# Optimization experiments

Hardware: AMD Instinct MI355X
Metric: run time of the kernel (lower is better)

The kernel has to match this reference:

```python
import jax, jax.numpy as jnp
import numpy as np

B, N, K = 2, 8192, 9
FEAT_C, COST_C, FLOW_C = 128, 64, 3
CH = [128, 128]          # PointConv output channels
MLP = [128, 64]          # pointwise Conv1d channels
WN = 16                  # WeightNet output width
HID = [8, 8]             # WeightNet hidden widths
SLOPE = 0.1              # leaky relu slope
EPS = 1e-5
CLAMP = (-200.0, 200.0)


def setup_inputs() -> dict:
    key = jax.random.key(0)
    ks = iter(jax.random.split(key, 64))
    def nrm(shape, s=0.02):
        return jax.random.normal(next(ks), shape, jnp.float32) * s
    inp = {}
    inp["xyz"] = jax.random.normal(next(ks), (B, N, 3), jnp.float32)
    inp["feats"] = jax.random.normal(next(ks), (B, FEAT_C, N), jnp.float32)
    inp["cost_volume"] = jax.random.normal(next(ks), (B, COST_C, N), jnp.float32)
    inp["flow"] = jax.random.normal(next(ks), (B, FLOW_C, N), jnp.float32)
    last = FEAT_C + COST_C + FLOW_C
    for i, co in enumerate(CH):
        cin = last + 3
        p = f"pc{i}_"
        inp[p + "w1"] = nrm((HID[0], 3)); inp[p + "b1"] = jnp.zeros((HID[0],), jnp.float32)
        inp[p + "w2"] = nrm((HID[1], HID[0])); inp[p + "b2"] = jnp.zeros((HID[1],), jnp.float32)
        inp[p + "w3"] = nrm((WN, HID[1])); inp[p + "b3"] = jnp.zeros((WN,), jnp.float32)
        inp[p + "linW"] = nrm((co, cin * WN)); inp[p + "linb"] = jnp.zeros((co,), jnp.float32)
        last = co
    for i, co in enumerate(MLP):
        inp[f"mlp{i}_W"] = nrm((co, last)); inp[f"mlp{i}_b"] = jnp.zeros((co,), jnp.float32)
        last = co
    inp["fc_W"] = nrm((3, last)); inp["fc_b"] = jnp.zeros((3,), jnp.float32)
    return inp


def _bn(x, axes):
    m = x.mean(axes, keepdims=True)
    v = x.var(axes, keepdims=True)
    return (x - m) / jnp.sqrt(v + EPS)


def _leaky(x):
    return jnp.where(x >= 0, x, SLOPE * x)


def _knn_idx(xyz, k):
    # xyz: [B,N,3] -> idx [B,N,K] of k nearest (incl. self)
    sq = jnp.sum(xyz * xyz, -1)                       # [B,N]
    d = sq[:, :, None] + sq[:, None, :] - 2.0 * jnp.einsum('bnc,bmc->bnm', xyz, xyz)
    return jax.lax.top_k(-d, k)[1]                    # [B,N,K]


def _gather(a, idx):
    # a: [B,N,C], idx: [B,N,K] -> [B,N,K,C]
    return jax.vmap(lambda x, i: x[i])(a, idx)


def _pointconv(xyz, points, idx, w1, b1, w2, b2, w3, b3, linW, linb):
    # xyz [B,N,3], points [B,C,N] -> [B,out,N]
    g_xyz = _gather(xyz, idx) - xyz[:, :, None, :]    # [B,N,K,3] relative coords
    g_pts = _gather(jnp.transpose(points, (0, 2, 1)), idx)  # [B,N,K,C]
    grouped = jnp.concatenate([g_pts, g_xyz], -1)     # [B,N,K,C+3]
    # WeightNet on relative coords: 3 -> 8 -> 8 -> 16 (bn+relu each)
    h = jax.nn.relu(_bn(g_xyz @ w1.T + b1, (0, 1, 2)))
    h = jax.nn.relu(_bn(h @ w2.T + b2, (0, 1, 2)))
    w = jax.nn.relu(_bn(h @ w3.T + b3, (0, 1, 2)))    # [B,N,K,WN]
    bsz, n = grouped.shape[0], grouped.shape[1]
    agg = jnp.einsum('bnkc,bnkw->bncw', grouped, w).reshape(bsz, n, -1)
    out = agg @ linW.T + linb                         # [B,N,out]
    out = _leaky(_bn(out, (0, 1)))
    return jnp.transpose(out, (0, 2, 1))              # [B,out,N]


def reference(xyz, feats, cost_volume, flow,
              pc0_w1, pc0_b1, pc0_w2, pc0_b2, pc0_w3, pc0_b3, pc0_linW, pc0_linb,
              pc1_w1, pc1_b1, pc1_w2, pc1_b2, pc1_w3, pc1_b3, pc1_linW, pc1_linb,
              mlp0_W, mlp0_b, mlp1_W, mlp1_b, fc_W, fc_b):
    idx = _knn_idx(xyz, K)
    x = jnp.concatenate([feats, cost_volume, flow], axis=1)  # [B, feat+cost+flow, N]
    x = _pointconv(xyz, x, idx, pc0_w1, pc0_b1, pc0_w2, pc0_b2, pc0_w3, pc0_b3, pc0_linW, pc0_linb)
    x = _pointconv(xyz, x, idx, pc1_w1, pc1_b1, pc1_w2, pc1_b2, pc1_w3, pc1_b3, pc1_linW, pc1_linb)
    x = _leaky(jnp.einsum('oc,bcn->bon', mlp0_W, x) + mlp0_b[None, :, None])
    x = _leaky(jnp.einsum('oc,bcn->bon', mlp1_W, x) + mlp1_b[None, :, None])
    fl = jnp.einsum('oc,bcn->bon', fc_W, x) + fc_b[None, :, None]
    return x, jnp.clip(fl, CLAMP[0], CLAMP[1])
```

## Files before the change

### kernel.cpp

```cpp
#include <hip/hip_runtime.h>

#define NBATCH 2
#define NPTS   8192
#define NPT    (NBATCH*NPTS)
#define KNN    9
#define SEG    16
#define SEGN   (NPTS/SEG)
#define SCAP   16
#define SSTR   17

typedef unsigned short u16;
typedef unsigned int   u32;
typedef short bf16x8 __attribute__((ext_vector_type(8)));
typedef float f32x4  __attribute__((ext_vector_type(4)));

__device__ __forceinline__ float wred(float v){
#pragma unroll
  for(int o=32;o>0;o>>=1) v += __shfl_down(v,o);
  return v;
}

__device__ __forceinline__ u16 f2b(float f){
  u32 u = __float_as_uint(f);
  return (u16)((u + 0x7fffu + ((u>>16)&1u)) >> 16);
}

__device__ __forceinline__ float bumpup(float x){
  u32 u = __float_as_uint(x);
  if(u == 0x80000000u) u = 1u;
  else if((int)u >= 0) u += 1u;
  else u -= 1u;
  return __uint_as_float(u);
}

__global__ __launch_bounds__(256) void k_build_xin(
    const float* __restrict__ feats, const float* __restrict__ cost,
    const float* __restrict__ flow, float* __restrict__ xin)
{
  __shared__ float buf[196][67];
  int t = threadIdx.x;
  int pt0 = blockIdx.x*64;
  int b = pt0 >> 13, n0 = pt0 & (NPTS-1);
  int lane = t & 63, grp = t >> 6;
  const float* f  = feats + (size_t)b*128*NPTS + n0 + lane;
  const float* cv = cost  + (size_t)b*64 *NPTS + n0 + lane;
  const float* fl = flow  + (size_t)b*3  *NPTS + n0 + lane;
  for(int c=grp; c<128; c+=4) buf[c][lane]      = f[(size_t)c*NPTS];
  for(int c=grp; c<64;  c+=4) buf[128+c][lane]  = cv[(size_t)c*NPTS];
  if(grp<3) buf[192+grp][lane] = fl[(size_t)grp*NPTS];
  else      buf[195][lane] = 0.f;
  __syncthreads();
  for(int e=t; e<64*49; e+=256){
    int p = e/49, q = e-p*49;
    float4 v = make_float4(buf[4*q][p], buf[4*q+1][p], buf[4*q+2][p], buf[4*q+3][p]);
    *(float4*)(xin + (size_t)(pt0+p)*196 + 4*q) = v;
  }
}

__global__ __launch_bounds__(256) void k_thr(
    const float* __restrict__ xyz, float* __restrict__ thr)
{
  __shared__ float md[4][64][9];
  int t = threadIdx.x, lane = t & 63, wave = t >> 6;
  int qb = blockIdx.x;
  int b = qb >> 7;
  int n = (qb & 127)*64 + lane;
  const float* xb = xyz + (size_t)b*NPTS*3;
  float qx=xb[3*n], qy=xb[3*n+1], qz=xb[3*n+2];
  float qs = __fadd_rn(__fadd_rn(__fmul_rn(qx,qx),__fmul_rn(qy,qy)),__fmul_rn(qz,qz));
  float bd[KNN];
#pragma unroll
  for(int i=0;i<KNN;i++) bd[i]=__builtin_inff();
  for(int i=0;i<128;i++){
    int m = (wave*128 + i)*16;
    float cx=xb[3*m], cy=xb[3*m+1], cz=xb[3*m+2];
    float s = __fadd_rn(__fadd_rn(__fmul_rn(cx,cx),__fmul_rn(cy,cy)),__fmul_rn(cz,cz));
    float dot = fmaf(cz,qz, fmaf(cy,qy, __fmul_rn(cx,qx)));
    float d = __fsub_rn(__fadd_rn(qs,s), __fmul_rn(2.0f,dot));
    if(d < bd[KNN-1]){
      bd[KNN-1]=d;
#pragma unroll
      for(int r=KNN-2;r>=0;r--){
        if(bd[r+1] < bd[r]){ float td=bd[r]; bd[r]=bd[r+1]; bd[r+1]=td; }
      }
    }
  }
#pragma unroll
  for(int i=0;i<KNN;i++) md[wave][lane][i]=bd[i];
  __syncthreads();
  if(t < 64){
    float b2[KNN];
#pragma unroll
    for(int i=0;i<KNN;i++) b2[i]=__builtin_inff();
    for(int w=0;w<4;w++){
#pragma unroll
      for(int i=0;i<KNN;i++){
        float d = md[w][t][i];
        if(d < b2[KNN-1]){
          b2[KNN-1]=d;
#pragma unroll
          for(int r=KNN-2;r>=0;r--){
            if(b2[r+1] < b2[r]){ float td=b2[r]; b2[r]=b2[r+1]; b2[r+1]=td; }
          }
        }
      }
    }
    thr[(b<<13) + (qb & 127)*64 + t] = b2[KNN-1];
  }
}

__global__ __launch_bounds__(256) void k_knn_part(
    const float* __restrict__ xyz, const float* __restrict__ thr,
    float* __restrict__ pd, int* __restrict__ pi)
{
  __shared__ float4 cbuf[256];
  __shared__ float sdq[256*SSTR];
  __shared__ int   sqi[256*SSTR];
  int t = threadIdx.x;
  int seg = blockIdx.x & (SEG-1);
  int qc  = blockIdx.x >> 4;
  int b = qc >> 5;
  int n = (qc & 31)*256 + t;
  int pt = (b<<13) + t + (qc&31)*256;
  pt = (b<<13) + n;
  const float* xb = xyz + (size_t)b*NPTS*3;
  float qx=xb[3*n], qy=xb[3*n+1], qz=xb[3*n+2];
  float qs = __fadd_rn(__fadd_rn(__fmul_rn(qx,qx),__fmul_rn(qy,qy)),__fmul_rn(qz,qz));
  float init = bumpup(thr[pt]);
  float bd[KNN]; int bi[KNN];
#pragma unroll
  for(int i=0;i<KNN;i++){ bd[i]=init; bi[i]=0x7fffffff; }
  float cut = init;
  int cnt = 0;
  float* msd = sdq + t*SSTR;
  int*   msi = sqi + t*SSTR;
  auto flush = [&](){
    for(int i=0;i<cnt;i++){
      float d = msd[i]; int id = msi[i];
      if(d < bd[KNN-1]){
        bd[KNN-1]=d; bi[KNN-1]=id;
#pragma unroll
        for(int r=KNN-2;r>=0;r--){
          if(bd[r+1] < bd[r]){
            float td=bd[r]; bd[r]=bd[r+1]; bd[r+1]=td;
            int ti=bi[r]; bi[r]=bi[r+1]; bi[r+1]=ti;
          }
        }
      }
    }
    cnt = 0;
    cut = bd[KNN-1];
  };
  const int m0 = seg*SEGN;
  for(int tt=0; tt<SEGN; tt+=256){
    int m = m0 + tt + t;
    float cx=xb[3*m], cy=xb[3*m+1], cz=xb[3*m+2];
    float s = __fadd_rn(__fadd_rn(__fmul_rn(cx,cx),__fmul_rn(cy,cy)),__fmul_rn(cz,cz));
    cbuf[t] = make_float4(cx,cy,cz,s);
    __syncthreads();
    for(int j0=0; j0<256; j0+=8){
      float dv[8];
#pragma unroll
      for(int u=0;u<8;u++){
        float4 c = cbuf[j0+u];
        float dot = fmaf(c.z,qz, fmaf(c.y,qy, __fmul_rn(c.x,qx)));
        dv[u] = __fsub_rn(__fadd_rn(qs,c.w), __fmul_rn(2.0f,dot));
      }
#pragma unroll
      for(int u=0;u<8;u++){
        msd[cnt] = dv[u];
        msi[cnt] = m0+tt+j0+u;
        cnt += (dv[u] < cut) ? 1 : 0;
      }
      if(cnt > 8) flush();
    }
    __syncthreads();
  }
  flush();
  size_t base = ((size_t)pt*SEG + seg)*KNN;
#pragma unroll
  for(int i=0;i<KNN;i++){ pd[base+i]=bd[i]; pi[base+i]=bi[i]; }
}

__global__ __launch_bounds__(256) void k_knn_merge(
    const float* __restrict__ xyz,
    const float* __restrict__ pd, const int* __restrict__ pi,
    int* __restrict__ idxo, float* __restrict__ gpart)
{
  __shared__ float red[4][9];
  int t = threadIdx.x;
  int pt = blockIdx.x*256 + t;
  int b = pt >> 13, n = pt & (NPTS-1);
  const float* xb = xyz + (size_t)b*NPTS*3;
  const float4* dp = (const float4*)(pd + (size_t)pt*SEG*KNN);
  const int4*   ip = (const int4*)(pi + (size_t)pt*SEG*KNN);
  float bd[KNN]; int bi[KNN];
#pragma unroll
  for(int i=0;i<KNN;i++){ bd[i]=__builtin_inff(); bi[i]=0x7fffffff; }
  for(int v=0; v<SEG*KNN/4; v++){
    float4 dv = dp[v];
    int4   iv = ip[v];
    float dd[4] = {dv.x,dv.y,dv.z,dv.w};
    int   ii[4] = {iv.x,iv.y,iv.z,iv.w};
#pragma unroll
    for(int u=0;u<4;u++){
      float d = dd[u]; int id = ii[u];
      if(d < bd[KNN-1]){
        bd[KNN-1]=d; bi[KNN-1]=id;
#pragma unroll
        for(int i=KNN-2;i>=0;i--){
          if(bd[i+1] < bd[i]){
            float td=bd[i]; bd[i]=bd[i+1]; bd[i+1]=td;
            int ti=bi[i]; bi[i]=bi[i+1]; bi[i+1]=ti;
          }
        }
      }
    }
  }
#pragma unroll
  for(int r=0;r<KNN;r++) idxo[pt*KNN + r] = bi[r];
  float q0=xb[3*n], q1=xb[3*n+1], q2=xb[3*n+2];
  float mom[9];
#pragma unroll
  for(int i=0;i<9;i++) mom[i]=0.f;
#pragma unroll
  for(int r=0;r<KNN;r++){
    int m = bi[r];
    float gx=xb[3*m]-q0, gy=xb[3*m+1]-q1, gz=xb[3*m+2]-q2;
    mom[0]+=gx; mom[1]+=gy; mom[2]+=gz;
    mom[3]=fmaf(gx,gx,mom[3]); mom[4]=fmaf(gy,gy,mom[4]); mom[5]=fmaf(gz,gz,mom[5]);
    mom[6]=fmaf(gx,gy,mom[6]); mom[7]=fmaf(gx,gz,mom[7]); mom[8]=fmaf(gy,gz,mom[8]);
  }
  int wave = t>>6, lane = t&63;
#pragma unroll
  for(int i=0;i<9;i++){
    float s = wred(mom[i]);
    if(lane==0) red[wave][i]=s;
  }
  __syncthreads();
  if(t<9)
    gpart[blockIdx.x*9 + t] = red[0][t]+red[1][t]+red[2][t]+red[3][t];
}

__global__ __launch_bounds__(256) void k_wn23a(
    const float* __restrict__ xyz, const int* __restrict__ idx,
    const float* __restrict__ gpart, float cnt,
    const float* __restrict__ W1, const float* __restrict__ B1,
    const float* __restrict__ W2, const float* __restrict__ B2,
    float* __restrict__ hout, float* __restrict__ partialOut)
{
  __shared__ float mom[9];
  __shared__ float stl[16];
  int t = threadIdx.x;
  if(t<9){
    float s=0.f;
    for(int r=0;r<64;r++) s += gpart[r*9+t];
    mom[t]=s;
  }
  __syncthreads();
  if(t<8){
    float inv = 1.0f/cnt;
    float w0=W1[3*t], w1=W1[3*t+1], w2=W1[3*t+2], bb=B1[t];
    float Eg0=mom[0]*inv, Eg1=mom[1]*inv, Eg2=mom[2]*inv;
    float Mxx=mom[3]*inv, Myy=mom[4]*inv, Mzz=mom[5]*inv;
    float Mxy=mom[6]*inv, Mxz=mom[7]*inv, Myz=mom[8]*inv;
    float mu_lin = w0*Eg0 + w1*Eg1 + w2*Eg2;
    float mean = mu_lin + bb;
    float e2 = w0*w0*Mxx + w1*w1*Myy + w2*w2*Mzz
             + 2.f*(w0*w1*Mxy + w0*w2*Mxz + w1*w2*Myz)
             + 2.f*bb*mu_lin + bb*bb;
    float var = e2 - mean*mean;
    stl[t] = mean;
    stl[8+t] = 1.0f/sqrtf(var + 1e-5f);
  }
  __syncthreads();
  int e = blockIdx.x*256 + t;
  int pt = e/KNN;
  int b = pt>>13, n = pt & (NPTS-1);
  int m = idx[e];
  const float* xb = xyz + (size_t)b*NPTS*3;
  float gx = xb[3*m]-xb[3*n], gy = xb[3*m+1]-xb[3*n+1], gz = xb[3*m+2]-xb[3*n+2];
  float x[8];
#pragma unroll
  for(int j=0;j<8;j++){
    float d = fmaf(gz, W1[3*j+2], fmaf(gy, W1[3*j+1], gx*W1[3*j]));
    float v = d + B1[j];
    v = (v - stl[j])*stl[8+j];
    x[j] = v>0.f? v : 0.f;
  }
  float v[8];
#pragma unroll
  for(int j=0;j<8;j++){
    float d = 0.f;
#pragma unroll
    for(int i=0;i<8;i++) d = fmaf(x[i], W2[j*8+i], d);
    v[j] = d + B2[j];
    hout[(size_t)e*8 + j] = v[j];
  }
  __shared__ float red[4][2][8];
  int wave = t>>6, lane = t&63;
#pragma unroll
  for(int j=0;j<8;j++){
    float s = wred(v[j]);
    float q = wred(v[j]*v[j]);
    if(lane==0){ red[wave][0][j]=s; red[wave][1][j]=q; }
  }
  __syncthreads();
  if(t < 16){
    int isq = t>>3, c = t&7;
    partialOut[blockIdx.x*16 + t] =
      red[0][isq][c]+red[1][isq][c]+red[2][isq][c]+red[3][isq][c];
  }
}

template<int CI, int CO>
__global__ __launch_bounds__(256) void k_wn23(
    const float* __restrict__ hin, const float* __restrict__ partialIn,
    int nb, float cnt,
    const float* __restrict__ W, const float* __restrict__ Bv,
    float* __restrict__ hout, float* __restrict__ partialOut)
{
  __shared__ float sa[256], qa[256];
  __shared__ float stl[2*CI];
  int t = threadIdx.x;
  {
    int c = t % CI;
    int r0 = t / CI;
    int stride = 256 / CI;
    float s=0.f, q=0.f;
    for(int r=r0; r<nb; r+=stride){
      s += partialIn[r*2*CI + c];
      q += partialIn[r*2*CI + CI + c];
    }
    sa[t]=s; qa[t]=q;
    __syncthreads();
    if(t < CI){
      for(int g=1; g<stride; g++){ s += sa[t+g*CI]; q += qa[t+g*CI]; }
      float mean = s/cnt;
      float var  = q/cnt - mean*mean;
      stl[t]    = mean;
      stl[CI+t] = 1.0f/sqrtf(var + 1e-5f);
    }
    __syncthreads();
  }
  int e = blockIdx.x*256 + t;
  float x[CI];
#pragma unroll
  for(int i=0;i<CI;i++){
    float v = (hin[(size_t)e*CI + i] - stl[i])*stl[CI+i];
    x[i] = v>0.f? v : 0.f;
  }
  float v[CO];
#pragma unroll
  for(int j=0;j<CO;j++){
    float d = 0.f;
#pragma unroll
    for(int i=0;i<CI;i++) d = fmaf(x[i], W[j*CI+i], d);
    v[j] = d + Bv[j];
    hout[(size_t)e*CO + j] = v[j];
  }
  __shared__ float red[4][2][CO];
  int wave = t>>6, lane = t&63;
#pragma unroll
  for(int j=0;j<CO;j++){
    float s = wred(v[j]);
    float q = wred(v[j]*v[j]);
    if(lane==0){ red[wave][0][j]=s; red[wave][1][j]=q; }
  }
  __syncthreads();
  if(t < 2*CO){
    int isq = t/CO, c = t%CO;
    partialOut[blockIdx.x*2*CO + t] =
      red[0][isq][c]+red[1][isq][c]+red[2][isq][c]+red[3][isq][c];
  }
}

__global__ __launch_bounds__(256) void k_fin(
    const float* __restrict__ partial, float* __restrict__ st,
    int C, int nb, float cnt)
{
  __shared__ float sa[256], qa[256];
  int t = threadIdx.x;
  int c = t % C;
  int r0 = t / C;
  int stride = 256 / C;
  float s=0.f, q=0.f;
  for(int r=r0; r<nb; r+=stride){
    s += partial[r*2*C + c];
    q += partial[r*2*C + C + c];
  }
  sa[t]=s; qa[t]=q;
  __syncthreads();
  if(t < C){
    for(int g=1; g<stride; g++){ s += sa[t+g*C]; q += qa[t+g*C]; }
    float mean = s/cnt;
    float var  = q/cnt - mean*mean;
    st[t]   = mean;
    st[C+t] = 1.0f/sqrtf(var + 1e-5f);
  }
}

__global__ __launch_bounds__(256) void k_prepW(
    const float* __restrict__ linW, u16* __restrict__ Wh, int AW, int KP)
{
  int e = blockIdx.x*256 + threadIdx.x;
  if(e >= 128*KP) return;
  int o = e / KP, k = e - o*KP;
  float w = (k < AW) ? linW[o*AW + k] : 0.f;
  Wh[e] = f2b(w);
}

template<int CIN, int XSTRIDE, int KP, bool BN>
__global__ __launch_bounds__(256) void k_buildA(
    const float* __restrict__ xin, const float* __restrict__ xyz,
    const int* __restrict__ idx, const float* __restrict__ wpre,
    const float* __restrict__ st3, const float* __restrict__ bnst,
    u16* __restrict__ Abuf, int c0)
{
  constexpr int P = 16;
  constexpr int CPTS = CIN-3;
  constexpr int CPAD = KP/16;
  __shared__ float wm[P][KNN][16];
  __shared__ float gxs[P][KNN][3];
  __shared__ int   si[P][KNN];
  __shared__ float sm3[16], sr3[16];
  int t = threadIdx.x;
  int pt0 = c0 + blockIdx.x*P;
  int b = pt0 >> 13;
  const float* xb = xyz + (size_t)b*NPTS*3;
  if(t<16){ sm3[t]=st3[t]; sr3[t]=st3[16+t]; }
  for(int e=t; e<P*KNN; e+=256){
    int p = e/KNN, k = e - p*KNN;
    int n = (pt0+p)&(NPTS-1);
    int m = idx[(pt0+p)*KNN+k];
    si[p][k]=m;
    gxs[p][k][0]=xb[3*m]  -xb[3*n];
    gxs[p][k][1]=xb[3*m+1]-xb[3*n+1];
    gxs[p][k][2]=xb[3*m+2]-xb[3*n+2];
  }
  __syncthreads();
  for(int e=t; e<P*KNN*16; e+=256){
    int p = e/(KNN*16); int r = e - p*(KNN*16); int k = r>>4, wn = r&15;
    float v = (wpre[((size_t)(pt0+p)*KNN + k)*16 + wn] - sm3[wn]) * sr3[wn];
    wm[p][k][wn] = v>0.f? v:0.f;
  }
  __syncthreads();
  for(int it=t; it<P*CPAD; it+=256){
    int p = it/CPAD, c = it - p*CPAD;
    u32 u[8];
    if(c < CIN){
      float g[KNN];
      if(c < CPTS){
#pragma unroll
        for(int k=0;k<KNN;k++)
          g[k] = xin[(size_t)((b<<13) + si[p][k])*XSTRIDE + c];
        if(BN){
          float sm = bnst[c], sr = bnst[128+c];
#pragma unroll
          for(int k=0;k<KNN;k++){
            float v = (g[k]-sm)*sr;
            g[k] = v>=0.f? v : 0.1f*v;
          }
        }
      } else {
        int cc = c - CPTS;
#pragma unroll
        for(int k=0;k<KNN;k++) g[k] = gxs[p][k][cc];
      }
      float a[16];
#pragma unroll
      for(int wn=0; wn<16; wn++){
        float s = 0.f;
#pragma unroll
        for(int k=0;k<KNN;k++) s = fmaf(g[k], wm[p][k][wn], s);
        a[wn] = s;
      }
#pragma unroll
      for(int j=0;j<8;j++)
        u[j] = (u32)f2b(a[2*j]) | ((u32)f2b(a[2*j+1])<<16);
    } else {
#pragma unroll
      for(int j=0;j<8;j++) u[j]=0;
    }
    u32* dst = (u32*)(Abuf + ((size_t)(blockIdx.x*P + p)*KP + c*16));
    *(uint4*)dst       = make_uint4(u[0],u[1],u[2],u[3]);
    *((uint4*)dst + 1) = make_uint4(u[4],u[5],u[6],u[7]);
  }
}

__device__ __forceinline__ void gload16(const void* g, void* l){
  __builtin_amdgcn_global_load_lds(
      (const __attribute__((address_space(1))) u32*)g,
      (__attribute__((address_space(3))) u32*)l, 16, 0, 0);
}

template<int KP>
__global__ __launch_bounds__(512) void k_gemm(
    const u16* __restrict__ Wh, const u16* __restrict__ A,
    const float* __restrict__ linb, float* __restrict__ outp,
    float* __restrict__ partial, int ptBase)
{
  __shared__ __attribute__((aligned(16))) u16 lds[24576];
  constexpr int NT = KP/64;
  int t = threadIdx.x, wave = t>>6, lane = t&63;
  int p0 = blockIdx.x*64;
  const u16* Ab = A + (size_t)p0*KP;

  auto stage = [&](const u16* __restrict__ g, int k0, int ldsByteOff, int rows){
    int nr = (rows*128) >> 13;
    for(int r=0;r<nr;r++){
      int y  = (r*8 + wave) << 10;
      int yl = y + lane*16;
      int row = yl >> 7;
      int s = (yl >> 4) & 7;
      int c = s ^ (row & 7);
      const u16* src = g + (size_t)row*KP + k0 + c*8;
      gload16(src, (char*)lds + ldsByteOff + y);
    }
  };

  stage(Wh, 0, 0,     128);
  stage(Ab, 0, 32768, 64);

  f32x4 acc[4];
#pragma unroll
  for(int j=0;j<4;j++) acc[j]=(f32x4)(0.f);

  for(int kt=0; kt<NT; kt++){
    int cur = kt & 1;
    __syncthreads();
    if(kt+1 < NT){
      int nxt = cur^1;
      stage(Wh, (kt+1)*64, nxt*16384,         128);
      stage(Ab, (kt+1)*64, 32768 + nxt*8192,  64);
    }
    const u16* Lw = lds + cur*8192;
    const u16* La = lds + 16384 + cur*4096;
#pragma unroll
    for(int kf=0; kf<2; kf++){
      int cb = kf*4 + (lane>>4);
      bf16x8 af[4];
#pragma unroll
      for(int nf=0; nf<4; nf++){
        int p = nf*16 + (lane&15);
        af[nf] = *(const bf16x8*)(La + p*64 + ((cb ^ (p&7))<<3));
      }
      int row = wave*16 + (lane&15);
      bf16x8 wh = *(const bf16x8*)(Lw + row*64 + ((cb ^ (row&7))<<3));
#pragma unroll
      for(int nf=0; nf<4; nf++)
        acc[nf] = __builtin_amdgcn_mfma_f32_16x16x32_bf16(wh, af[nf], acc[nf], 0,0,0);
    }
  }

  int gb = (ptBase>>6) + blockIdx.x;
  int q = lane>>4, lc = lane&15;
  int obase = wave*16 + q*4;
#pragma unroll
  for(int r=0;r<4;r++){
    int o = obase + r;
    float bo = linb[o];
    float sv = 0.f, qv = 0.f;
#pragma unroll
    for(int nf=0; nf<4; nf++){
      float x = acc[nf][r] + bo;
      outp[(size_t)(ptBase + p0 + nf*16 + lc)*128 + o] = x;
      sv += x; qv = fmaf(x,x,qv);
    }
#pragma unroll
    for(int off=8; off>0; off>>=1){
      sv += __shfl_down(sv,off);
      qv += __shfl_down(qv,off);
    }
    if(lc==0){
      partial[gb*256 + o]       = sv;
      partial[gb*256 + 128 + o] = qv;
    }
  }
}

__global__ __launch_bounds__(512) void k_mlp(
    const float* __restrict__ outp1, const float* __restrict__ sto,
    const float* __restrict__ W0, const float* __restrict__ B0,
    const float* __restrict__ W1, const float* __restrict__ B1,
    const float* __restrict__ Wf, const float* __restrict__ Bf,
    float* __restrict__ dout)
{
  __shared__ float w0l[128*129];
  __shared__ float w1l[128*65];
  __shared__ float xt [128*65];
  __shared__ float m1l[64*65];
  int t = threadIdx.x;
  int pt0 = blockIdx.x*64;
  int b = pt0 >> 13, n0 = pt0 & (NPTS-1);
  for(int e=t; e<128*128; e+=512){ int o=e>>7, j=e&127; w0l[j*129+o] = W0[e]; }
  for(int e=t; e<64*128;  e+=512){ int o=e>>7, j=e&127; w1l[j*65+o]  = W1[e]; }
  for(int e=t; e<64*128;  e+=512){
    int p=e>>7, j=e&127;
    float v = outp1[(size_t)(pt0+p)*128 + j];
    v = (v - sto[j])*sto[128+j];
    xt[j*65+p] = v>=0.f? v : 0.1f*v;
  }
  __syncthreads();
  int p = t&63, wv = t>>6;
  float acc[16];
#pragma unroll
  for(int i=0;i<16;i++) acc[i]=0.f;
  for(int j=0;j<128;j++){
    float xv = xt[j*65+p];
#pragma unroll
    for(int i=0;i<16;i++)
      acc[i] = fmaf(w0l[j*129 + wv*16 + i], xv, acc[i]);
  }
  __syncthreads();
#pragma unroll
  for(int i=0;i<16;i++){
    int o = wv*16+i;
    float v = acc[i] + B0[o];
    v = v>=0.f? v : 0.1f*v;
    xt[o*65 + p] = v;
  }
  __syncthreads();
  float a2[8];
#pragma unroll
  for(int i=0;i<8;i++) a2[i]=0.f;
  for(int j=0;j<128;j++){
    float xv = xt[j*65+p];
#pragma unroll
    for(int i=0;i<8;i++)
      a2[i] = fmaf(w1l[j*65 + wv*8 + i], xv, a2[i]);
  }
#pragma unroll
  for(int i=0;i<8;i++){
    int o = wv*8+i;
    float v = a2[i] + B1[o];
    v = v>=0.f? v : 0.1f*v;
    dout[(size_t)(b*64+o)*NPTS + n0 + p] = v;
    m1l[o*65+p] = v;
  }
  __syncthreads();
  if(t < 192){
    int o = t/64, pp = t%64;
    float a = Bf[o];
    for(int j=0;j<64;j++) a = fmaf(Wf[o*64+j], m1l[j*65+pp], a);
    a = fminf(fmaxf(a, -200.f), 200.f);
    dout[(size_t)NBATCH*64*NPTS + (size_t)(b*3+o)*NPTS + n0 + pp] = a;
  }
}

extern "C" void kernel_launch(void* const* d_in, const int* in_sizes, int n_in,
                              void* d_out, int out_size, void* d_ws, size_t ws_size,
                              hipStream_t stream)
{
  (void)in_sizes; (void)n_in; (void)out_size;
  const float* xyz   = (const float*)d_in[0];
  const float* feats = (const float*)d_in[1];
  const float* cost  = (const float*)d_in[2];
  const float* flow  = (const float*)d_in[3];
  const float* pw1[2]  = {(const float*)d_in[4],  (const float*)d_in[12]};
  const float* pb1[2]  = {(const float*)d_in[5],  (const float*)d_in[13]};
  const float* pw2[2]  = {(const float*)d_in[6],  (const float*)d_in[14]};
  const float* pb2[2]  = {(const float*)d_in[7],  (const float*)d_in[15]};
  const float* pw3[2]  = {(const float*)d_in[8],  (const float*)d_in[16]};
  const float* pb3[2]  = {(const float*)d_in[9],  (const float*)d_in[17]};
  const float* plW[2]  = {(const float*)d_in[10], (const float*)d_in[18]};
  const float* plb[2]  = {(const float*)d_in[11], (const float*)d_in[19]};
  const float* m0W = (const float*)d_in[20];
  const float* m0b = (const float*)d_in[21];
  const float* m1W = (const float*)d_in[22];
  const float* m1b = (const float*)d_in[23];
  const float* fcW = (const float*)d_in[24];
  const float* fcb = (const float*)d_in[25];
  float* out = (float*)d_out;

  const int KP0 = 3200, AW0 = 3168;
  const int KP1 = 2112, AW1 = 2096;

  float* ws = (float*)d_ws;
  size_t o = 0;
  float* xin0 = ws + o; o += (size_t)NPT*196;
  int*   idx  = (int*)(ws + o); o += (size_t)NPT*KNN + 3;
  o &= ~(size_t)3;
  float* thr  = ws + o; o += (size_t)NPT;
  float* pd   = ws + o; o += (size_t)NPT*SEG*KNN;
  int*   pi   = (int*)(ws + o); o += (size_t)NPT*SEG*KNN;
  float* h2   = ws + o; o += (size_t)NPT*KNN*8;
  float* wpre = ws + o; o += (size_t)NPT*KNN*16;
  float* gpart = ws + o; o += 64*9 + 7;
  float* part2 = ws + o; o += 576*16;
  float* part3 = ws + o; o += 576*32;
  float* parto = ws + o; o += 65536;
  float* st3  = ws + o; o += 32;
  float* sto0 = ws + o; o += 256;
  float* sto1 = ws + o; o += 256;
  float* outp0 = ws + o; o += (size_t)NPT*128;
  float* outp1 = ws + o; o += (size_t)NPT*128;
  u16* Wh0 = (u16*)(ws + o); o += (size_t)128*KP0/2;
  u16* Wh1 = (u16*)(ws + o); o += (size_t)128*KP1/2;
  u16* Abuf = (u16*)(ws + o);
  size_t used_bytes = o*4;
  size_t avail = ws_size > used_bytes ? ws_size - used_bytes : 0;
  int npc = NPT;
  while(npc > 1024 && (size_t)npc*KP0*2 > avail) npc >>= 1;

  k_build_xin<<<NPT/64, 256, 0, stream>>>(feats, cost, flow, xin0);
  k_thr<<<256, 256, 0, stream>>>(xyz, thr);
  k_knn_part<<<64*SEG, 256, 0, stream>>>(xyz, thr, pd, pi);
  k_knn_merge<<<NPT/256, 256, 0, stream>>>(xyz, pd, pi, idx, gpart);

  k_prepW<<<(128*KP0+255)/256, 256, 0, stream>>>(plW[0], Wh0, AW0, KP0);
  k_prepW<<<(128*KP1+255)/256, 256, 0, stream>>>(plW[1], Wh1, AW1, KP1);

  const float cnt1 = (float)(NPT*KNN);
  const float cnto = (float)NPT;

  for(int L=0; L<2; ++L){
    k_wn23a<<<576,256,0,stream>>>(xyz, idx, gpart, cnt1,
                                  pw1[L], pb1[L], pw2[L], pb2[L], h2, part2);
    k_wn23<8,16><<<576,256,0,stream>>>(h2, part2, 576, cnt1, pw3[L], pb3[L], wpre, part3);
    k_fin<<<1,256,0,stream>>>(part3, st3, 16, 576, cnt1);
    for(int c0 = 0; c0 < NPT; c0 += npc){
      if(L==0){
        k_buildA<198,196,KP0,false><<<npc/16,256,0,stream>>>(xin0, xyz, idx, wpre, st3, sto0, Abuf, c0);
        k_gemm<KP0><<<npc/64,512,0,stream>>>(Wh0, Abuf, plb[0], outp0, parto, c0);
      } else {
        k_buildA<131,128,KP1,true><<<npc/16,256,0,stream>>>(outp0, xyz, idx, wpre, st3, sto0, Abuf, c0);
        k_gemm<KP1><<<npc/64,512,0,stream>>>(Wh1, Abuf, plb[1], outp1, parto, c0);
      }
    }
    k_fin<<<1,256,0,stream>>>(parto, (L==0)? sto0 : sto1, 128, NPT/64, cnto);
  }

  k_mlp<<<NPT/64,512,0,stream>>>(outp1, sto1, m0W,m0b, m1W,m1b, fcW,fcb, out);
}
```

Baseline: 566.4 us.

## Precompute packed xyz+norm, read candidates directly in KNN, batch both WeightNet layers

A new pass packs each point's coordinates and squared norm into a float4 array. The threshold and partial-KNN kernels now read from it instead of recomputing norms, and the partial KNN drops its shared-memory candidate staging and block barriers in favour of direct global (L1/L2-cached) float4 loads. Its candidate buffering also changes to append only on a hit, flushing when the buffer is full. Separately, the WeightNet stages for both PointConv layers are fused into single launches with separate buffers, cutting the number of kernel launches and small reductions from six to three.

```diff
diff --git a/kernel.cpp b/kernel.cpp
--- a/kernel.cpp
+++ b/kernel.cpp
@@ -57,26 +57,36 @@
   }
 }
 
+__global__ __launch_bounds__(256) void k_xyzs(
+    const float* __restrict__ xyz, float4* __restrict__ xs)
+{
+  int pt = blockIdx.x*256 + threadIdx.x;
+  int b = pt >> 13, n = pt & (NPTS-1);
+  const float* p = xyz + (size_t)b*NPTS*3 + 3*n;
+  float x=p[0], y=p[1], z=p[2];
+  float s = __fadd_rn(__fadd_rn(__fmul_rn(x,x),__fmul_rn(y,y)),__fmul_rn(z,z));
+  xs[pt] = make_float4(x,y,z,s);
+}
+
 __global__ __launch_bounds__(256) void k_thr(
-    const float* __restrict__ xyz, float* __restrict__ thr)
+    const float4* __restrict__ xs, float* __restrict__ thr)
 {
   __shared__ float md[4][64][9];
   int t = threadIdx.x, lane = t & 63, wave = t >> 6;
   int qb = blockIdx.x;
   int b = qb >> 7;
   int n = (qb & 127)*64 + lane;
-  const float* xb = xyz + (size_t)b*NPTS*3;
-  float qx=xb[3*n], qy=xb[3*n+1], qz=xb[3*n+2];
-  float qs = __fadd_rn(__fadd_rn(__fmul_rn(qx,qx),__fmul_rn(qy,qy)),__fmul_rn(qz,qz));
+  const float4* xb4 = xs + (size_t)b*NPTS;
+  float4 q = xb4[n];
+  float qx=q.x, qy=q.y, qz=q.z, qs=q.w;
   float bd[KNN];
 #pragma unroll
   for(int i=0;i<KNN;i++) bd[i]=__builtin_inff();
   for(int i=0;i<128;i++){
     int m = (wave*128 + i)*16;
-    float cx=xb[3*m], cy=xb[3*m+1], cz=xb[3*m+2];
-    float s = __fadd_rn(__fadd_rn(__fmul_rn(cx,cx),__fmul_rn(cy,cy)),__fmul_rn(cz,cz));
-    float dot = fmaf(cz,qz, fmaf(cy,qy, __fmul_rn(cx,qx)));
-    float d = __fsub_rn(__fadd_rn(qs,s), __fmul_rn(2.0f,dot));
+    float4 c = xb4[m];
+    float dot = fmaf(c.z,qz, fmaf(c.y,qy, __fmul_rn(c.x,qx)));
+    float d = __fsub_rn(__fadd_rn(qs,c.w), __fmul_rn(2.0f,dot));
     if(d < bd[KNN-1]){
       bd[KNN-1]=d;
 #pragma unroll
@@ -110,10 +120,9 @@
 }
 
 __global__ __launch_bounds__(256) void k_knn_part(
-    const float* __restrict__ xyz, const float* __restrict__ thr,
+    const float4* __restrict__ xs, const float* __restrict__ thr,
     float* __restrict__ pd, int* __restrict__ pi)
 {
-  __shared__ float4 cbuf[256];
   __shared__ float sdq[256*SSTR];
   __shared__ int   sqi[256*SSTR];
   int t = threadIdx.x;
@@ -121,11 +130,10 @@
   int qc  = blockIdx.x >> 4;
   int b = qc >> 5;
   int n = (qc & 31)*256 + t;
-  int pt = (b<<13) + t + (qc&31)*256;
-  pt = (b<<13) + n;
-  const float* xb = xyz + (size_t)b*NPTS*3;
-  float qx=xb[3*n], qy=xb[3*n+1], qz=xb[3*n+2];
-  float qs = __fadd_rn(__fadd_rn(__fmul_rn(qx,qx),__fmul_rn(qy,qy)),__fmul_rn(qz,qz));
+  int pt = (b<<13) + n;
+  const float4* xb4 = xs + (size_t)b*NPTS;
+  float4 q = xb4[n];
+  float qx=q.x, qy=q.y, qz=q.z, qs=q.w;
   float init = bumpup(thr[pt]);
   float bd[KNN]; int bi[KNN];
 #pragma unroll
@@ -152,29 +160,21 @@
     cut = bd[KNN-1];
   };
   const int m0 = seg*SEGN;
-  for(int tt=0; tt<SEGN; tt+=256){
-    int m = m0 + tt + t;
-    float cx=xb[3*m], cy=xb[3*m+1], cz=xb[3*m+2];
-    float s = __fadd_rn(__fadd_rn(__fmul_rn(cx,cx),__fmul_rn(cy,cy)),__fmul_rn(cz,cz));
-    cbuf[t] = make_float4(cx,cy,cz,s);
-    __syncthreads();
-    for(int j0=0; j0<256; j0+=8){
-      float dv[8];
-#pragma unroll
-      for(int u=0;u<8;u++){
-        float4 c = cbuf[j0+u];
-        float dot = fmaf(c.z,qz, fmaf(c.y,qy, __fmul_rn(c.x,qx)));
-        dv[u] = __fsub_rn(__fadd_rn(qs,c.w), __fmul_rn(2.0f,dot));
-      }
-#pragma unroll
-      for(int u=0;u<8;u++){
-        msd[cnt] = dv[u];
-        msi[cnt] = m0+tt+j0+u;
-        cnt += (dv[u] < cut) ? 1 : 0;
-      }
-      if(cnt > 8) flush();
-    }
-    __syncthreads();
+  for(int j0=0; j0<SEGN; j0+=8){
+    float dv[8];
+#pragma unroll
+    for(int u=0;u<8;u++){
+      float4 c = xb4[m0+j0+u];
+      float dot = fmaf(c.z,qz, fmaf(c.y,qy, __fmul_rn(c.x,qx)));
+      dv[u] = __fsub_rn(__fadd_rn(qs,c.w), __fmul_rn(2.0f,dot));
+    }
+#pragma unroll
+    for(int u=0;u<8;u++){
+      if(dv[u] < cut){
+        msd[cnt]=dv[u]; msi[cnt]=m0+j0+u; cnt++;
+        if(cnt==SCAP) flush();
+      }
+    }
   }
   flush();
   size_t base = ((size_t)pt*SEG + seg)*KNN;
@@ -242,15 +242,19 @@
     gpart[blockIdx.x*9 + t] = red[0][t]+red[1][t]+red[2][t]+red[3][t];
 }
 
-__global__ __launch_bounds__(256) void k_wn23a(
+__global__ __launch_bounds__(256) void k_wn23a2(
     const float* __restrict__ xyz, const int* __restrict__ idx,
     const float* __restrict__ gpart, float cnt,
-    const float* __restrict__ W1, const float* __restrict__ B1,
-    const float* __restrict__ W2, const float* __restrict__ B2,
-    float* __restrict__ hout, float* __restrict__ partialOut)
+    const float* __restrict__ W1a, const float* __restrict__ B1a,
+    const float* __restrict__ W2a, const float* __restrict__ B2a,
+    const float* __restrict__ W1b, const float* __restrict__ B1b,
+    const float* __restrict__ W2b, const float* __restrict__ B2b,
+    float* __restrict__ houta, float* __restrict__ houtb,
+    float* __restrict__ parta, float* __restrict__ partb)
 {
   __shared__ float mom[9];
-  __shared__ float stl[16];
+  __shared__ float stl[2][16];
+  __shared__ float red[4][2][8];
   int t = threadIdx.x;
   if(t<9){
     float s=0.f;
@@ -258,9 +262,12 @@
     mom[t]=s;
   }
   __syncthreads();
-  if(t<8){
+  if(t<16){
+    int L = t>>3, j = t&7;
+    const float* W1 = L? W1b : W1a;
+    const float* B1 = L? B1b : B1a;
     float inv = 1.0f/cnt;
-    float w0=W1[3*t], w1=W1[3*t+1], w2=W1[3*t+2], bb=B1[t];
+    float w0=W1[3*j], w1=W1[3*j+1], w2=W1[3*j+2], bb=B1[j];
     float Eg0=mom[0]*inv, Eg1=mom[1]*inv, Eg2=mom[2]*inv;
     float Mxx=mom[3]*inv, Myy=mom[4]*inv, Mzz=mom[5]*inv;
     float Mxy=mom[6]*inv, Mxz=mom[7]*inv, Myz=mom[8]*inv;
@@ -270,8 +277,8 @@
              + 2.f*(w0*w1*Mxy + w0*w2*Mxz + w1*w2*Myz)
              + 2.f*bb*mu_lin + bb*bb;
     float var = e2 - mean*mean;
-    stl[t] = mean;
-    stl[8+t] = 1.0f/sqrtf(var + 1e-5f);
+    stl[L][j] = mean;
+    stl[L][8+j] = 1.0f/sqrtf(var + 1e-5f);
   }
   __syncthreads();
   int e = blockIdx.x*256 + t;
@@ -280,98 +287,150 @@
   int m = idx[e];
   const float* xb = xyz + (size_t)b*NPTS*3;
   float gx = xb[3*m]-xb[3*n], gy = xb[3*m+1]-xb[3*n+1], gz = xb[3*m+2]-xb[3*n+2];
-  float x[8];
-#pragma unroll
-  for(int j=0;j<8;j++){
-    float d = fmaf(gz, W1[3*j+2], fmaf(gy, W1[3*j+1], gx*W1[3*j]));
-    float v = d + B1[j];
-    v = (v - stl[j])*stl[8+j];
-    x[j] = v>0.f? v : 0.f;
-  }
-  float v[8];
-#pragma unroll
-  for(int j=0;j<8;j++){
-    float d = 0.f;
-#pragma unroll
-    for(int i=0;i<8;i++) d = fmaf(x[i], W2[j*8+i], d);
-    v[j] = d + B2[j];
-    hout[(size_t)e*8 + j] = v[j];
-  }
-  __shared__ float red[4][2][8];
   int wave = t>>6, lane = t&63;
 #pragma unroll
-  for(int j=0;j<8;j++){
-    float s = wred(v[j]);
-    float q = wred(v[j]*v[j]);
-    if(lane==0){ red[wave][0][j]=s; red[wave][1][j]=q; }
-  }
-  __syncthreads();
-  if(t < 16){
-    int isq = t>>3, c = t&7;
-    partialOut[blockIdx.x*16 + t] =
-      red[0][isq][c]+red[1][isq][c]+red[2][isq][c]+red[3][isq][c];
-  }
-}
-
-template<int CI, int CO>
-__global__ __launch_bounds__(256) void k_wn23(
-    const float* __restrict__ hin, const float* __restrict__ partialIn,
+  for(int L=0; L<2; L++){
+    const float* W1 = L? W1b : W1a;
+    const float* B1 = L? B1b : B1a;
+    const float* W2 = L? W2b : W2a;
+    const float* B2 = L? B2b : B2a;
+    float* hout = L? houtb : houta;
+    float* part = L? partb : parta;
+    float x[8];
+#pragma unroll
+    for(int j=0;j<8;j++){
+      float d = fmaf(gz, W1[3*j+2], fmaf(gy, W1[3*j+1], gx*W1[3*j]));
+      float v = d + B1[j];
+      v = (v - stl[L][j])*stl[L][8+j];
+      x[j] = v>0.f? v : 0.f;
+    }
+    float v[8];
+#pragma unroll
+    for(int j=0;j<8;j++){
+      float d = 0.f;
+#pragma unroll
+      for(int i=0;i<8;i++) d = fmaf(x[i], W2[j*8+i], d);
+      v[j] = d + B2[j];
+      hout[(size_t)e*8 + j] = v[j];
+    }
+#pragma unroll
+    for(int j=0;j<8;j++){
+      float s = wred(v[j]);
+      float q = wred(v[j]*v[j]);
+      if(lane==0){ red[wave][0][j]=s; red[wave][1][j]=q; }
+    }
+    __syncthreads();
+    if(t < 16){
+      int isq = t>>3, c = t&7;
+      part[blockIdx.x*16 + t] =
+        red[0][isq][c]+red[1][isq][c]+red[2][isq][c]+red[3][isq][c];
+    }
+    __syncthreads();
+  }
+}
+
+__global__ __launch_bounds__(256) void k_wn23_2(
+    const float* __restrict__ hina, const float* __restrict__ pina,
+    const float* __restrict__ hinb, const float* __restrict__ pinb,
     int nb, float cnt,
-    const float* __restrict__ W, const float* __restrict__ Bv,
-    float* __restrict__ hout, float* __restrict__ partialOut)
+    const float* __restrict__ Wa, const float* __restrict__ Ba,
+    const float* __restrict__ Wb, const float* __restrict__ Bb,
+    float* __restrict__ houta, float* __restrict__ houtb,
+    float* __restrict__ parta, float* __restrict__ partb)
 {
   __shared__ float sa[256], qa[256];
-  __shared__ float stl[2*CI];
+  __shared__ float stl[16];
+  __shared__ float red[4][2][16];
   int t = threadIdx.x;
-  {
-    int c = t % CI;
-    int r0 = t / CI;
-    int stride = 256 / CI;
+  int e = blockIdx.x*256 + t;
+  int wave = t>>6, lane = t&63;
+#pragma unroll
+  for(int L=0; L<2; L++){
+    const float* hin = L? hinb : hina;
+    const float* pin = L? pinb : pina;
+    const float* W   = L? Wb : Wa;
+    const float* Bv  = L? Bb : Ba;
+    float* hout = L? houtb : houta;
+    float* part = L? partb : parta;
+    {
+      int c = t % 8;
+      int r0 = t / 8;
+      float s=0.f, q=0.f;
+      for(int r=r0; r<nb; r+=32){
+        s += pin[r*16 + c];
+        q += pin[r*16 + 8 + c];
+      }
+      sa[t]=s; qa[t]=q;
+      __syncthreads();
+      if(t < 8){
+        for(int g=1; g<32; g++){ s += sa[t+g*8]; q += qa[t+g*8]; }
+        float mean = s/cnt;
+        float var  = q/cnt - mean*mean;
+        stl[t]   = mean;
+        stl[8+t] = 1.0f/sqrtf(var + 1e-5f);
+      }
+      __syncthreads();
+    }
+    float x[8];
+#pragma unroll
+    for(int i=0;i<8;i++){
+      float v = (hin[(size_t)e*8 + i] - stl[i])*stl[8+i];
+      x[i] = v>0.f? v : 0.f;
+    }
+    float v[16];
+#pragma unroll
+    for(int j=0;j<16;j++){
+      float d = 0.f;
+#pragma unroll
+      for(int i=0;i<8;i++) d = fmaf(x[i], W[j*8+i], d);
+      v[j] = d + Bv[j];
+      hout[(size_t)e*16 + j] = v[j];
+    }
+#pragma unroll
+    for(int j=0;j<16;j++){
+      float s = wred(v[j]);
+      float q = wred(v[j]*v[j]);
+      if(lane==0){ red[wave][0][j]=s; red[wave][1][j]=q; }
+    }
+    __syncthreads();
+    if(t < 32){
+      int isq = t>>4, c = t&15;
+      part[blockIdx.x*32 + t] =
+        red[0][isq][c]+red[1][isq][c]+red[2][isq][c]+red[3][isq][c];
+    }
+    __syncthreads();
+  }
+}
+
+__global__ __launch_bounds__(256) void k_fin2(
+    const float* __restrict__ pa, const float* __restrict__ pb,
+    float* __restrict__ sta, float* __restrict__ stb, int nb, float cnt)
+{
+  __shared__ float sa[256], qa[256];
+  int t = threadIdx.x;
+  const int C = 16;
+#pragma unroll
+  for(int L=0; L<2; L++){
+    const float* partial = L? pb : pa;
+    float* st = L? stb : sta;
+    int c = t % C;
+    int r0 = t / C;
+    int stride = 256 / C;
     float s=0.f, q=0.f;
     for(int r=r0; r<nb; r+=stride){
-      s += partialIn[r*2*CI + c];
-      q += partialIn[r*2*CI + CI + c];
+      s += partial[r*2*C + c];
+      q += partial[r*2*C + C + c];
     }
     sa[t]=s; qa[t]=q;
     __syncthreads();
-    if(t < CI){
-      for(int g=1; g<stride; g++){ s += sa[t+g*CI]; q += qa[t+g*CI]; }
+    if(t < C){
+      for(int g=1; g<stride; g++){ s += sa[t+g*C]; q += qa[t+g*C]; }
       float mean = s/cnt;
       float var  = q/cnt - mean*mean;
-      stl[t]    = mean;
-      stl[CI+t] = 1.0f/sqrtf(var + 1e-5f);
+      st[t]   = mean;
+      st[C+t] = 1.0f/sqrtf(var + 1e-5f);
     }
     __syncthreads();
-  }
-  int e = blockIdx.x*256 + t;
-  float x[CI];
-#pragma unroll
-  for(int i=0;i<CI;i++){
-    float v = (hin[(size_t)e*CI + i] - stl[i])*stl[CI+i];
-    x[i] = v>0.f? v : 0.f;
-  }
-  float v[CO];
-#pragma unroll
-  for(int j=0;j<CO;j++){
-    float d = 0.f;
-#pragma unroll
-    for(int i=0;i<CI;i++) d = fmaf(x[i], W[j*CI+i], d);
-    v[j] = d + Bv[j];
-    hout[(size_t)e*CO + j] = v[j];
-  }
-  __shared__ float red[4][2][CO];
-  int wave = t>>6, lane = t&63;
-#pragma unroll
-  for(int j=0;j<CO;j++){
-    float s = wred(v[j]);
-    float q = wred(v[j]*v[j]);
-    if(lane==0){ red[wave][0][j]=s; red[wave][1][j]=q; }
-  }
-  __syncthreads();
-  if(t < 2*CO){
-    int isq = t/CO, c = t%CO;
-    partialOut[blockIdx.x*2*CO + t] =
-      red[0][isq][c]+red[1][isq][c]+red[2][isq][c]+red[3][isq][c];
   }
 }
 
@@ -681,16 +740,22 @@
   float* xin0 = ws + o; o += (size_t)NPT*196;
   int*   idx  = (int*)(ws + o); o += (size_t)NPT*KNN + 3;
   o &= ~(size_t)3;
+  float4* xs  = (float4*)(ws + o); o += (size_t)NPT*4;
   float* thr  = ws + o; o += (size_t)NPT;
   float* pd   = ws + o; o += (size_t)NPT*SEG*KNN;
   int*   pi   = (int*)(ws + o); o += (size_t)NPT*SEG*KNN;
-  float* h2   = ws + o; o += (size_t)NPT*KNN*8;
-  float* wpre = ws + o; o += (size_t)NPT*KNN*16;
+  float* h2a  = ws + o; o += (size_t)NPT*KNN*8;
+  float* h2b  = ws + o; o += (size_t)NPT*KNN*8;
+  float* wpre0 = ws + o; o += (size_t)NPT*KNN*16;
+  float* wpre1 = ws + o; o += (size_t)NPT*KNN*16;
   float* gpart = ws + o; o += 64*9 + 7;
-  float* part2 = ws + o; o += 576*16;
-  float* part3 = ws + o; o += 576*32;
+  float* part2a = ws + o; o += 576*16;
+  float* part2b = ws + o; o += 576*16;
+  float* part3a = ws + o; o += 576*32;
+  float* part3b = ws + o; o += 576*32;
   float* parto = ws + o; o += 65536;
-  float* st3  = ws + o; o += 32;
+  float* st3a = ws + o; o += 32;
+  float* st3b = ws + o; o += 32;
   float* sto0 = ws + o; o += 256;
   float* sto1 = ws + o; o += 256;
   float* outp0 = ws + o; o += (size_t)NPT*128;
@@ -704,8 +769,9 @@
   while(npc > 1024 && (size_t)npc*KP0*2 > avail) npc >>= 1;
 
   k_build_xin<<<NPT/64, 256, 0, stream>>>(feats, cost, flow, xin0);
-  k_thr<<<256, 256, 0, stream>>>(xyz, thr);
-  k_knn_part<<<64*SEG, 256, 0, stream>>>(xyz, thr, pd, pi);
+  k_xyzs<<<NPT/256, 256, 0, stream>>>(xyz, xs);
+  k_thr<<<256, 256, 0, stream>>>(xs, thr);
+  k_knn_part<<<64*SEG, 256, 0, stream>>>(xs, thr, pd, pi);
   k_knn_merge<<<NPT/256, 256, 0, stream>>>(xyz, pd, pi, idx, gpart);
 
   k_prepW<<<(128*KP0+255)/256, 256, 0, stream>>>(plW[0], Wh0, AW0, KP0);
@@ -714,22 +780,26 @@
   const float cnt1 = (float)(NPT*KNN);
   const float cnto = (float)NPT;
 
-  for(int L=0; L<2; ++L){
-    k_wn23a<<<576,256,0,stream>>>(xyz, idx, gpart, cnt1,
-                                  pw1[L], pb1[L], pw2[L], pb2[L], h2, part2);
-    k_wn23<8,16><<<576,256,0,stream>>>(h2, part2, 576, cnt1, pw3[L], pb3[L], wpre, part3);
-    k_fin<<<1,256,0,stream>>>(part3, st3, 16, 576, cnt1);
-    for(int c0 = 0; c0 < NPT; c0 += npc){
-      if(L==0){
-        k_buildA<198,196,KP0,false><<<npc/16,256,0,stream>>>(xin0, xyz, idx, wpre, st3, sto0, Abuf, c0);
-        k_gemm<KP0><<<npc/64,512,0,stream>>>(Wh0, Abuf, plb[0], outp0, parto, c0);
-      } else {
-        k_buildA<131,128,KP1,true><<<npc/16,256,0,stream>>>(outp0, xyz, idx, wpre, st3, sto0, Abuf, c0);
-        k_gemm<KP1><<<npc/64,512,0,stream>>>(Wh1, Abuf, plb[1], outp1, parto, c0);
-      }
-    }
-    k_fin<<<1,256,0,stream>>>(parto, (L==0)? sto0 : sto1, 128, NPT/64, cnto);
-  }
+  k_wn23a2<<<576,256,0,stream>>>(xyz, idx, gpart, cnt1,
+                                 pw1[0], pb1[0], pw2[0], pb2[0],
+                                 pw1[1], pb1[1], pw2[1], pb2[1],
+                                 h2a, h2b, part2a, part2b);
+  k_wn23_2<<<576,256,0,stream>>>(h2a, part2a, h2b, part2b, 576, cnt1,
+                                 pw3[0], pb3[0], pw3[1], pb3[1],
+                                 wpre0, wpre1, part3a, part3b);
+  k_fin2<<<1,256,0,stream>>>(part3a, part3b, st3a, st3b, 576, cnt1);
+
+  for(int c0 = 0; c0 < NPT; c0 += npc){
+    k_buildA<198,196,KP0,false><<<npc/16,256,0,stream>>>(xin0, xyz, idx, wpre0, st3a, sto0, Abuf, c0);
+    k_gemm<KP0><<<npc/64,512,0,stream>>>(Wh0, Abuf, plb[0], outp0, parto, c0);
+  }
+  k_fin<<<1,256,0,stream>>>(parto, sto0, 128, NPT/64, cnto);
+
+  for(int c0 = 0; c0 < NPT; c0 += npc){
+    k_buildA<131,128,KP1,true><<<npc/16,256,0,stream>>>(outp0, xyz, idx, wpre1, st3b, sto0, Abuf, c0);
+    k_gemm<KP1><<<npc/64,512,0,stream>>>(Wh1, Abuf, plb[1], outp1, parto, c0);
+  }
+  k_fin<<<1,256,0,stream>>>(parto, sto1, 128, NPT/64, cnto);
 
   k_mlp<<<NPT/64,512,0,stream>>>(outp1, sto1, m0W,m0b, m1W,m1b, fcW,fcb, out);
 }
```

After: 543.1 us. 1.04x faster.
